# Optimization experiments

Measured on AMD Instinct MI355X. Metric: run time of the kernel, lower is better.

Reference implementation:

```python
import jax, jax.numpy as jnp
import numpy as np


def setup_inputs() -> dict:
    key = jax.random.key(0)
    k1, k2 = jax.random.split(key)
    pc1 = jax.random.normal(k1, (8, 2048, 3), dtype=jnp.float32)
    pc2 = jax.random.normal(k2, (8, 2048, 3), dtype=jnp.float32)
    return {"pc1": pc1, "pc2": pc2}


def reference(pc1, pc2):
    # Flatten to point lists, matching pc.reshape(-1, 3)
    p1 = pc1.reshape(-1, 3)  # [N1, 3]
    p2 = pc2.reshape(-1, 3)  # [N2, 3]
    # Squared pairwise distances via ||a||^2 + ||b||^2 - 2 a.b
    sq1 = jnp.sum(p1 * p1, axis=-1)  # [N1]
    sq2 = jnp.sum(p2 * p2, axis=-1)  # [N2]
    d2 = sq1[:, None] + sq2[None, :] - 2.0 * jnp.einsum('nd,md->nm', p1, p2)  # [N1, N2]
    d2 = jnp.maximum(d2, 0.0)
    d = jnp.sqrt(d2)  # Euclidean, matching cKDTree.query distances
    # dist1 = NN distance from each pc2 point into pc1 (tree1.query(pc2))
    dist1 = jnp.min(d, axis=0)  # [N2]
    # dist2 = NN distance from each pc1 point into pc2 (tree2.query(pc1))
    dist2 = jnp.min(d, axis=1)  # [N1]
    return jnp.mean(dist1) + jnp.mean(dist2)
```

## Files before the change

kernel.cpp:

```cpp
#include <hip/hip_runtime.h>
#include <math.h>

#define N_PTS 16384
#define TPB   256
#define IP    8
#define ROWS_B (TPB * IP)
#define IBLK  (N_PTS / ROWS_B)
#define JT    128
#define JS    (N_PTS / JT)
#define NCH   (JT / 2)
#define REDB  64

typedef float f32x2 __attribute__((ext_vector_type(2)));
typedef float f32x4 __attribute__((ext_vector_type(4)));

#define PK_ADD2(dst, a, b)                                                 \
  asm("v_pk_add_f32 %0, %1, %2" : "=v"(dst) : "v"(a), "v"(b))
#define PK_FMA2A(acc, a, b)                                                \
  asm("v_pk_fma_f32 %0, %1, %2, %0" : "+v"(acc) : "v"(a), "v"(b))
#define MIN3A(acc, a, b)                                                   \
  asm("v_min3_f32 %0, %1, %2, %0" : "+v"(acc) : "v"(a), "v"(b))

#define XDPP(v, CTRL)                                                      \
  v = __int_as_float(__builtin_amdgcn_update_dpp(                          \
      0, __float_as_int(v), CTRL, 0xF, 0xF, true))
#define XSWZ(v)                                                            \
  v = __int_as_float(__builtin_amdgcn_ds_swizzle(__float_as_int(v), 0x101F))

__global__ __launch_bounds__(TPB, 4) void chamfer_min(
    const float* __restrict__ p1, const float* __restrict__ p2,
    unsigned int* __restrict__ dmin, float* __restrict__ outp) {
  __shared__ f32x4 pkA[NCH];
  __shared__ f32x4 pkB[NCH];
  __shared__ unsigned int cmin[JT];

  if (blockIdx.x == 0 && blockIdx.y == 0 && threadIdx.x == 0)
    outp[0] = 0.f;

  const int jbase = blockIdx.x * JT;
  if (threadIdx.x < NCH) {
    int t = threadIdx.x;
    int ja = jbase + t, jb = jbase + t + NCH;
    float xa = p2[3 * ja], ya = p2[3 * ja + 1], za = p2[3 * ja + 2];
    float xb = p2[3 * jb], yb = p2[3 * jb + 1], zb = p2[3 * jb + 2];
    pkA[t] = (f32x4){xa, xb, ya, yb};
    pkB[t] = (f32x4){za, zb, 0.5f * (xa * xa + ya * ya + za * za),
                             0.5f * (xb * xb + yb * yb + zb * zb)};
  }
  if (threadIdx.x < JT) cmin[threadIdx.x] = 0x7F800000u;

  const int ibase = blockIdx.y * ROWS_B;
  f32x2 nx2[IP], ny2[IP], nz2[IP], h2[IP];
  float rmin[IP];
#pragma unroll
  for (int m = 0; m < IP; ++m) {
    int r = ibase + m * TPB + threadIdx.x;
    float x = p1[3 * r + 0], y = p1[3 * r + 1], z = p1[3 * r + 2];
    nx2[m] = (f32x2){-x, -x};
    ny2[m] = (f32x2){-y, -y};
    nz2[m] = (f32x2){-z, -z};
    float h = 0.5f * (x * x + y * y + z * z);
    h2[m] = (f32x2){h, h};
    rmin[m] = INFINITY;
  }
  __syncthreads();

  const int lane = threadIdx.x & 63;
  const int base = lane ^ ((threadIdx.x >> 6) << 4);
  int pos = base;
  float Aa = INFINITY, Ab = INFINITY;
  f32x4 qA, qB;

#define BODY()                                                             \
  {                                                                        \
    f32x2 X = qA.xy, Y = qA.zw, Z = qB.xy, W = qB.zw;                      \
    _Pragma("unroll")                                                      \
    for (int m = 0; m < IP; m += 2) {                                      \
      f32x2 s0, s1;                                                        \
      PK_ADD2(s0, h2[m], W);                                               \
      PK_FMA2A(s0, nx2[m], X);                                             \
      PK_FMA2A(s0, ny2[m], Y);                                             \
      PK_FMA2A(s0, nz2[m], Z);                                             \
      PK_ADD2(s1, h2[m + 1], W);                                           \
      PK_FMA2A(s1, nx2[m + 1], X);                                         \
      PK_FMA2A(s1, ny2[m + 1], Y);                                         \
      PK_FMA2A(s1, nz2[m + 1], Z);                                         \
      MIN3A(rmin[m],     s0.x, s0.y);                                      \
      MIN3A(rmin[m + 1], s1.x, s1.y);                                      \
      MIN3A(Aa, s0.x, s1.x);                                               \
      MIN3A(Ab, s0.y, s1.y);                                               \
    }                                                                      \
  }
#define SUBSTEP(D)                                                         \
  {                                                                        \
    if ((D) == 1)      { XDPP(Aa, 0xB1); XDPP(Ab, 0xB1); }                 \
    else if ((D) == 2) { XDPP(Aa, 0x4E); XDPP(Ab, 0x4E); }                 \
    else               { XSWZ(Aa);       XSWZ(Ab); }                       \
    pos ^= (D);                                                            \
    qA = pkA[pos]; qB = pkB[pos];                                          \
    BODY();                                                                \
  }

#pragma unroll 1
  for (int t = 0; t < 8; ++t) {
    if (t) {
      const int dh = 8 << __builtin_ctz(t);
      Aa = __shfl_xor(Aa, dh, 64);
      Ab = __shfl_xor(Ab, dh, 64);
      pos ^= dh;
    }
    qA = pkA[pos]; qB = pkB[pos];
    BODY();
    SUBSTEP(1); SUBSTEP(2); SUBSTEP(1); SUBSTEP(4);
    SUBSTEP(1); SUBSTEP(2); SUBSTEP(1);
  }

  atomicMin(&cmin[pos],       __float_as_uint(fmaxf(Aa, 0.f)));
  atomicMin(&cmin[pos + NCH], __float_as_uint(fmaxf(Ab, 0.f)));

#pragma unroll
  for (int m = 0; m < IP; ++m) {
    float d2 = fmaxf(0.f, 2.f * rmin[m]);
    atomicMin(&dmin[ibase + m * TPB + threadIdx.x], __float_as_uint(d2));
  }

  __syncthreads();
  for (int t = threadIdx.x; t < JT; t += TPB) {
    float v = __uint_as_float(cmin[t]);
    atomicMin(&dmin[N_PTS + jbase + t], __float_as_uint(2.f * v));
  }
}

__global__ __launch_bounds__(TPB) void chamfer_reduce(
    const unsigned int* __restrict__ dmin, float* __restrict__ outp) {
  float s = 0.f;
  for (int i = blockIdx.x * TPB + threadIdx.x; i < 2 * N_PTS; i += REDB * TPB)
    s += sqrtf(__uint_as_float(dmin[i]));
#pragma unroll
  for (int off = 32; off > 0; off >>= 1)
    s += __shfl_down(s, off, 64);
  __shared__ float partial[TPB / 64];
  if ((threadIdx.x & 63) == 0) partial[threadIdx.x >> 6] = s;
  __syncthreads();
  if (threadIdx.x == 0) {
    float t = 0.f;
    for (int w = 0; w < TPB / 64; ++w) t += partial[w];
    atomicAdd(outp, t * (1.0f / (float)N_PTS));
  }
}

extern "C" void kernel_launch(void* const* d_in, const int* in_sizes, int n_in,
                              void* d_out, int out_size, void* d_ws, size_t ws_size,
                              hipStream_t stream) {
  const float* pc1 = (const float*)d_in[0];
  const float* pc2 = (const float*)d_in[1];
  unsigned int* dmin = (unsigned int*)d_ws;

  chamfer_min<<<dim3(JS, IBLK), TPB, 0, stream>>>(pc1, pc2, dmin, (float*)d_out);
  chamfer_reduce<<<REDB, TPB, 0, stream>>>(dmin, (float*)d_out);
}
```

Baseline: 87.35 us.

## Prefetch next LDS tile, use scalar FMAs, halve rows per thread

Replaces packed FP32 FMA arithmetic with scalar fmaf and defers the per-row norm term until after the row minimum. Software-prefetches the next shared-memory point pair before computing the current one and moves the cross-lane exchange after the body. Halves rows per thread and doubles the occupancy target to hide latency. The scalar path issues more VALU instructions per pair, and the smaller per-thread tile lowers register-level reuse.

```diff
diff --git a/kernel.cpp b/kernel.cpp
--- a/kernel.cpp
+++ b/kernel.cpp
@@ -3,7 +3,7 @@
 
 #define N_PTS 16384
 #define TPB   256
-#define IP    8
+#define IP    4
 #define ROWS_B (TPB * IP)
 #define IBLK  (N_PTS / ROWS_B)
 #define JT    128
@@ -11,23 +11,17 @@
 #define NCH   (JT / 2)
 #define REDB  64
 
-typedef float f32x2 __attribute__((ext_vector_type(2)));
 typedef float f32x4 __attribute__((ext_vector_type(4)));
 
-#define PK_ADD2(dst, a, b)                                                 \
-  asm("v_pk_add_f32 %0, %1, %2" : "=v"(dst) : "v"(a), "v"(b))
-#define PK_FMA2A(acc, a, b)                                                \
-  asm("v_pk_fma_f32 %0, %1, %2, %0" : "+v"(acc) : "v"(a), "v"(b))
 #define MIN3A(acc, a, b)                                                   \
   asm("v_min3_f32 %0, %1, %2, %0" : "+v"(acc) : "v"(a), "v"(b))
-
 #define XDPP(v, CTRL)                                                      \
   v = __int_as_float(__builtin_amdgcn_update_dpp(                          \
       0, __float_as_int(v), CTRL, 0xF, 0xF, true))
 #define XSWZ(v)                                                            \
   v = __int_as_float(__builtin_amdgcn_ds_swizzle(__float_as_int(v), 0x101F))
 
-__global__ __launch_bounds__(TPB, 4) void chamfer_min(
+__global__ __launch_bounds__(TPB, 8) void chamfer_min(
     const float* __restrict__ p1, const float* __restrict__ p2,
     unsigned int* __restrict__ dmin, float* __restrict__ outp) {
   __shared__ f32x4 pkA[NCH];
@@ -50,17 +44,13 @@
   if (threadIdx.x < JT) cmin[threadIdx.x] = 0x7F800000u;
 
   const int ibase = blockIdx.y * ROWS_B;
-  f32x2 nx2[IP], ny2[IP], nz2[IP], h2[IP];
-  float rmin[IP];
+  float nx[IP], ny[IP], nz[IP], h[IP], rmin[IP];
 #pragma unroll
   for (int m = 0; m < IP; ++m) {
     int r = ibase + m * TPB + threadIdx.x;
     float x = p1[3 * r + 0], y = p1[3 * r + 1], z = p1[3 * r + 2];
-    nx2[m] = (f32x2){-x, -x};
-    ny2[m] = (f32x2){-y, -y};
-    nz2[m] = (f32x2){-z, -z};
-    float h = 0.5f * (x * x + y * y + z * z);
-    h2[m] = (f32x2){h, h};
+    nx[m] = -x; ny[m] = -y; nz[m] = -z;
+    h[m] = 0.5f * (x * x + y * y + z * z);
     rmin[m] = INFINITY;
   }
   __syncthreads();
@@ -69,50 +59,55 @@
   const int base = lane ^ ((threadIdx.x >> 6) << 4);
   int pos = base;
   float Aa = INFINITY, Ab = INFINITY;
-  f32x4 qA, qB;
+  f32x4 qA = pkA[pos], qB = pkB[pos], nqA, nqB;
 
 #define BODY()                                                             \
   {                                                                        \
-    f32x2 X = qA.xy, Y = qA.zw, Z = qB.xy, W = qB.zw;                      \
+    float Xa = qA.x, Xb = qA.y, Ya = qA.z, Yb = qA.w;                      \
+    float Za = qB.x, Zb = qB.y, Ca = qB.z, Cb = qB.w;                      \
     _Pragma("unroll")                                                      \
     for (int m = 0; m < IP; m += 2) {                                      \
-      f32x2 s0, s1;                                                        \
-      PK_ADD2(s0, h2[m], W);                                               \
-      PK_FMA2A(s0, nx2[m], X);                                             \
-      PK_FMA2A(s0, ny2[m], Y);                                             \
-      PK_FMA2A(s0, nz2[m], Z);                                             \
-      PK_ADD2(s1, h2[m + 1], W);                                           \
-      PK_FMA2A(s1, nx2[m + 1], X);                                         \
-      PK_FMA2A(s1, ny2[m + 1], Y);                                         \
-      PK_FMA2A(s1, nz2[m + 1], Z);                                         \
-      MIN3A(rmin[m],     s0.x, s0.y);                                      \
-      MIN3A(rmin[m + 1], s1.x, s1.y);                                      \
-      MIN3A(Aa, s0.x, s1.x);                                               \
-      MIN3A(Ab, s0.y, s1.y);                                               \
+      float ta = fmaf(nx[m], Xa, Ca);                                      \
+      ta = fmaf(ny[m], Ya, ta); ta = fmaf(nz[m], Za, ta);                  \
+      float tb = fmaf(nx[m], Xb, Cb);                                      \
+      tb = fmaf(ny[m], Yb, tb); tb = fmaf(nz[m], Zb, tb);                  \
+      float ua = fmaf(nx[m + 1], Xa, Ca);                                  \
+      ua = fmaf(ny[m + 1], Ya, ua); ua = fmaf(nz[m + 1], Za, ua);          \
+      float ub = fmaf(nx[m + 1], Xb, Cb);                                  \
+      ub = fmaf(ny[m + 1], Yb, ub); ub = fmaf(nz[m + 1], Zb, ub);          \
+      MIN3A(rmin[m],     ta, tb);                       \
+      MIN3A(rmin[m + 1], ua, ub);                                         \
+      MIN3A(Aa, ta + h[m], ua + h[m + 1]);              \
+      MIN3A(Ab, tb + h[m], ub + h[m + 1]);                                 \
     }                                                                      \
   }
-#define SUBSTEP(D)                                                         \
+#define SUB(D, XCH)                                                        \
   {                                                                        \
-    if ((D) == 1)      { XDPP(Aa, 0xB1); XDPP(Ab, 0xB1); }                 \
-    else if ((D) == 2) { XDPP(Aa, 0x4E); XDPP(Ab, 0x4E); }                 \
-    else               { XSWZ(Aa);       XSWZ(Ab); }                       \
-    pos ^= (D);                                                            \
-    qA = pkA[pos]; qB = pkB[pos];                                          \
+    const int np = pos ^ (D);                                              \
+    nqA = pkA[np]; nqB = pkB[np];                                          \
     BODY();                                                                \
+    XCH;                                                                   \
+    pos = np; qA = nqA; qB = nqB;                                          \
   }
+#define X1 { XDPP(Aa, 0xB1); XDPP(Ab, 0xB1); }
+#define X2 { XDPP(Aa, 0x4E); XDPP(Ab, 0x4E); }
+#define X4 { XSWZ(Aa); XSWZ(Ab); }
 
 #pragma unroll 1
   for (int t = 0; t < 8; ++t) {
-    if (t) {
-      const int dh = 8 << __builtin_ctz(t);
+    SUB(1, X1); SUB(2, X2); SUB(1, X1); SUB(4, X4);
+    SUB(1, X1); SUB(2, X2); SUB(1, X1);
+    if (t < 7) {
+      const int dh = 8 << __builtin_ctz(t + 1);
+      const int np = pos ^ dh;
+      nqA = pkA[np]; nqB = pkB[np];
+      BODY();
       Aa = __shfl_xor(Aa, dh, 64);
       Ab = __shfl_xor(Ab, dh, 64);
-      pos ^= dh;
+      pos = np; qA = nqA; qB = nqB;
+    } else {
+      BODY();
     }
-    qA = pkA[pos]; qB = pkB[pos];
-    BODY();
-    SUBSTEP(1); SUBSTEP(2); SUBSTEP(1); SUBSTEP(4);
-    SUBSTEP(1); SUBSTEP(2); SUBSTEP(1);
   }
 
   atomicMin(&cmin[pos],       __float_as_uint(fmaxf(Aa, 0.f)));
@@ -120,7 +115,7 @@
 
 #pragma unroll
   for (int m = 0; m < IP; ++m) {
-    float d2 = fmaxf(0.f, 2.f * rmin[m]);
+    float d2 = fmaxf(0.f, 2.f * (h[m] + rmin[m]));
     atomicMin(&dmin[ibase + m * TPB + threadIdx.x], __float_as_uint(d2));
   }
 
```

New measurement: 89.09 us. Within noise of the previous version (+2.0%).
